# Optimization experiments

Hardware: AMD Instinct MI355X
Metric: run time of the kernel (lower is better)

The kernel has to match this reference:

```python
import jax, jax.numpy as jnp
import numpy as np

FIELD_DIMS = [100000, 50000, 1000, 500, 100, 50, 20, 10]
INPUT_DIM = sum(FIELD_DIMS)            # 151680
NUM_FIELDS = len(FIELD_DIMS)           # 8
FACTOR_DIM = 16
HIDDEN = [256, 128]
OFFSETS = np.concatenate([[0], np.cumsum(FIELD_DIMS)[:-1]]).astype(np.int32)
BATCH = 2048
EPS = 1e-5


def setup_inputs() -> dict:
    key = jax.random.key(0)
    ks = jax.random.split(key, 32)
    # per-field indices, each within its own cardinality
    x = jnp.stack([
        jax.random.randint(ks[f], (BATCH,), 0, FIELD_DIMS[f], dtype=jnp.int32)
        for f in range(NUM_FIELDS)
    ], axis=1)  # [B, F]
    # concatenated embedding tables (xavier_uniform per torch init, approximated with uniform)
    lim = float(np.sqrt(6.0 / (max(FIELD_DIMS) + FACTOR_DIM)))
    emb_table = jax.random.uniform(ks[8], (INPUT_DIM, FACTOR_DIM), minval=-lim, maxval=lim, dtype=jnp.float32)
    # FM linear: weight ~ N(0, 0.01), bias 0
    w_lin = 0.01 * jax.random.normal(ks[9], (INPUT_DIM,), dtype=jnp.float32)
    b_lin = jnp.zeros((), dtype=jnp.float32)
    d0 = NUM_FIELDS * FACTOR_DIM  # 128
    def lin(k, fan_in, fan_out):
        b = float(np.sqrt(1.0 / fan_in))
        kw, kb = jax.random.split(k)
        W = jax.random.uniform(kw, (fan_in, fan_out), minval=-b, maxval=b, dtype=jnp.float32)
        bias = jax.random.uniform(kb, (fan_out,), minval=-b, maxval=b, dtype=jnp.float32)
        return W, bias
    W1, b1 = lin(ks[10], d0, HIDDEN[0])
    W2, b2 = lin(ks[11], HIDDEN[0], HIDDEN[1])
    W3, b3 = lin(ks[12], HIDDEN[1], 1)
    g1 = jnp.ones((HIDDEN[0],), jnp.float32); be1 = jnp.zeros((HIDDEN[0],), jnp.float32)
    g2 = jnp.ones((HIDDEN[1],), jnp.float32); be2 = jnp.zeros((HIDDEN[1],), jnp.float32)
    return {"x": x, "emb_table": emb_table, "w_lin": w_lin, "b_lin": b_lin,
            "W1": W1, "b1": b1, "g1": g1, "be1": be1,
            "W2": W2, "b2": b2, "g2": g2, "be2": be2,
            "W3": W3, "b3": b3}


def _batchnorm(h, gamma, beta):
    # training-mode BN (torch default): biased batch variance
    m = jnp.mean(h, axis=0)
    v = jnp.mean((h - m) ** 2, axis=0)
    return gamma * (h - m) / jnp.sqrt(v + EPS) + beta


def reference(x, emb_table, w_lin, b_lin, W1, b1, g1, be1, W2, b2, g2, be2, W3, b3):
    B = x.shape[0]
    offsets = jnp.asarray(OFFSETS)
    # --- faithful to original bug: scatter one-hot uses RAW x (no field offsets) ---
    sparse_x = jnp.zeros((B, INPUT_DIM), jnp.float32).at[
        jnp.arange(B)[:, None], x].set(1.0)  # duplicates collapse to 1.0, like scatter_
    y_linear = sparse_x @ w_lin + b_lin  # [B]
    # --- dense field embeddings (offset gather into concatenated table) ---
    dense_x = emb_table[x + offsets[None, :]]  # [B, F, K]
    s = jnp.sum(dense_x, axis=1)               # [B, K]
    square_of_sum = s * s
    sum_of_square = jnp.sum(dense_x * dense_x, axis=1)
    y_pairwise = 0.5 * jnp.sum(square_of_sum - sum_of_square, axis=1)  # [B]
    y_fm = y_linear + y_pairwise
    # --- DNN on concatenated embeddings ---
    h = dense_x.reshape(B, NUM_FIELDS * FACTOR_DIM)
    h = jax.nn.relu(_batchnorm(h @ W1 + b1, g1, be1))
    h = jax.nn.relu(_batchnorm(h @ W2 + b2, g2, be2))
    y_dnn = (h @ W3 + b3)[:, 0]  # [B]
    return y_fm + y_dnn
```

## Files before the change

### kernel.cpp

```cpp
#include <hip/hip_runtime.h>

#define EPS 1e-5f

static __device__ const int OFFS[8] = {0, 100000, 150000, 151000, 151500, 151600, 151650, 151670};

__global__ __launch_bounds__(256) void k1_gather_fm_gemm1(
    const int* __restrict__ x, const float* __restrict__ emb,
    const float* __restrict__ wlin, const float* __restrict__ blin,
    const float* __restrict__ W1, const float* __restrict__ b1,
    float* __restrict__ yfm, float* __restrict__ z1, float* __restrict__ p1)
{
    __shared__ __align__(16) float h0s[8][128];
    __shared__ __align__(16) float redS[8][128];
    __shared__ __align__(16) float redQ[8][128];

    const int t = threadIdx.x;
    const int rt = blockIdx.x >> 1, ch = blockIdx.x & 1;

    {
        const int r = t >> 5, c = t & 31;
        const int row = rt * 8 + r;
        const int f = c >> 2, dq = (c & 3) * 4;
        const int idxf = x[row * 8 + f];
        float4 e = *(const float4*)&emb[(size_t)(idxf + OFFS[f]) * 16 + dq];
        *(float4*)&h0s[r][f * 16 + dq] = e;

        if (ch == 0) {
            float4 s = e;
            float4 q = make_float4(e.x * e.x, e.y * e.y, e.z * e.z, e.w * e.w);
#pragma unroll
            for (int m = 4; m <= 16; m <<= 1) {
                s.x += __shfl_xor(s.x, m); s.y += __shfl_xor(s.y, m);
                s.z += __shfl_xor(s.z, m); s.w += __shfl_xor(s.w, m);
                q.x += __shfl_xor(q.x, m); q.y += __shfl_xor(q.y, m);
                q.z += __shfl_xor(q.z, m); q.w += __shfl_xor(q.w, m);
            }
            float pair = (s.x * s.x - q.x) + (s.y * s.y - q.y)
                       + (s.z * s.z - q.z) + (s.w * s.w - q.w);
            pair += __shfl_xor(pair, 1);
            pair += __shfl_xor(pair, 2);

            float lin = 0.f;
            if (c < 8) {
                int ids[8];
#pragma unroll
                for (int g = 0; g < 8; ++g) ids[g] = x[row * 8 + g];
                bool dup = false;
                for (int g = 0; g < c; ++g) dup = dup || (ids[g] == ids[c]);
                lin = dup ? 0.f : wlin[ids[c]];
            }
            lin += __shfl_xor(lin, 1);
            lin += __shfl_xor(lin, 2);
            lin += __shfl_xor(lin, 4);
            if (c == 0) yfm[row] = 0.5f * pair + lin + blin[0];
        }
    }
    __syncthreads();

    const int cc = t & 63, rg = t >> 6;
    const int j = ch * 128 + cc * 2;
    const int r0 = rg * 2;
    float a00 = 0.f, a01 = 0.f, a10 = 0.f, a11 = 0.f;
#pragma unroll
    for (int k0 = 0; k0 < 128; k0 += 16) {
        float4 ha[4], hb[4];
#pragma unroll
        for (int i = 0; i < 4; ++i) {
            ha[i] = *(const float4*)&h0s[r0][k0 + i * 4];
            hb[i] = *(const float4*)&h0s[r0 + 1][k0 + i * 4];
        }
        float2 w[16];
#pragma unroll
        for (int kk = 0; kk < 16; ++kk)
            w[kk] = *(const float2*)&W1[(size_t)(k0 + kk) * 256 + j];
#pragma unroll
        for (int kk = 0; kk < 16; ++kk) {
            const float hva = ((const float*)ha)[kk];
            const float hvb = ((const float*)hb)[kk];
            a00 += hva * w[kk].x; a01 += hva * w[kk].y;
            a10 += hvb * w[kk].x; a11 += hvb * w[kk].y;
        }
    }
    float2 b2v = *(const float2*)&b1[j];
    float z00 = a00 + b2v.x, z01 = a01 + b2v.y;
    float z10 = a10 + b2v.x, z11 = a11 + b2v.y;
    *(float2*)&z1[(size_t)(rt * 8 + r0) * 256 + j]     = make_float2(z00, z01);
    *(float2*)&z1[(size_t)(rt * 8 + r0 + 1) * 256 + j] = make_float2(z10, z11);
    *(float2*)&redS[r0][cc * 2]     = make_float2(z00, z01);
    *(float2*)&redS[r0 + 1][cc * 2] = make_float2(z10, z11);
    *(float2*)&redQ[r0][cc * 2]     = make_float2(z00 * z00, z01 * z01);
    *(float2*)&redQ[r0 + 1][cc * 2] = make_float2(z10 * z10, z11 * z11);
    __syncthreads();
    if (t < 128) {
        float s = 0.f, q = 0.f;
#pragma unroll
        for (int rr = 0; rr < 8; ++rr) { s += redS[rr][t]; q += redQ[rr][t]; }
        *(float2*)&p1[(size_t)(rt * 256 + ch * 128 + t) * 2] = make_float2(s, q);
    }
}

template <int NCOLS>
__global__ __launch_bounds__(256) void kr_stats(
    const float* __restrict__ p, const float* __restrict__ gamma,
    const float* __restrict__ beta, float* __restrict__ sg)
{
    __shared__ float partS[4][8], partQ[4][8];
    const int t = threadIdx.x, blk = blockIdx.x;
    const int cc = t & 7, g = t >> 3;
    const int col = blk * 8 + cc;

    float s = 0.f, q = 0.f;
#pragma unroll
    for (int i = 0; i < 8; ++i) {
        float2 v = *(const float2*)&p[(size_t)((g + i * 32) * NCOLS + col) * 2];
        s += v.x; q += v.y;
    }
#pragma unroll
    for (int m = 8; m <= 32; m <<= 1) {
        s += __shfl_xor(s, m);
        q += __shfl_xor(q, m);
    }
    if ((t & 63) < 8) {
        partS[t >> 6][cc] = s;
        partQ[t >> 6][cc] = q;
    }
    __syncthreads();
    if (t < 8) {
        float fs = partS[0][t] + partS[1][t] + partS[2][t] + partS[3][t];
        float fq = partQ[0][t] + partQ[1][t] + partQ[2][t] + partQ[3][t];
        const int c = blk * 8 + t;
        float mean = fs * (1.f / 2048.f);
        float var  = fq * (1.f / 2048.f) - mean * mean;
        float sc = gamma[c] * __frsqrt_rn(var + EPS);
        sg[c] = sc;
        sg[NCOLS + c] = beta[c] - mean * sc;
    }
}

__global__ __launch_bounds__(512) void k2_bn1_gemm2(
    const float* __restrict__ z1, const float* __restrict__ s1g,
    const float* __restrict__ W2, const float* __restrict__ b2,
    float* __restrict__ z2, float* __restrict__ p2)
{
    __shared__ __align__(16) float h1s[8][256];
    __shared__ __align__(16) float redS[8][128];
    __shared__ __align__(16) float redQ[8][128];

    const int t = threadIdx.x, blk = blockIdx.x;

    {
        const int lr = t >> 6, lc = (t & 63) * 4;
        float4 zv = *(const float4*)&z1[(size_t)(blk * 8 + lr) * 256 + lc];
        float4 sc = *(const float4*)&s1g[lc];
        float4 sh = *(const float4*)&s1g[256 + lc];
        float4 hv;
        hv.x = fmaxf(zv.x * sc.x + sh.x, 0.f);
        hv.y = fmaxf(zv.y * sc.y + sh.y, 0.f);
        hv.z = fmaxf(zv.z * sc.z + sh.z, 0.f);
        hv.w = fmaxf(zv.w * sc.w + sh.w, 0.f);
        *(float4*)&h1s[lr][lc] = hv;
    }
    __syncthreads();

    const int r = t >> 6, j = (t & 63) * 2;
    float a0 = 0.f, a1 = 0.f;
#pragma unroll
    for (int k0 = 0; k0 < 256; k0 += 16) {
        float4 h[4];
#pragma unroll
        for (int i = 0; i < 4; ++i) h[i] = *(const float4*)&h1s[r][k0 + i * 4];
        float2 w[16];
#pragma unroll
        for (int kk = 0; kk < 16; ++kk)
            w[kk] = *(const float2*)&W2[(size_t)(k0 + kk) * 128 + j];
#pragma unroll
        for (int kk = 0; kk < 16; ++kk) {
            const float hv = ((const float*)h)[kk];
            a0 += hv * w[kk].x; a1 += hv * w[kk].y;
        }
    }
    float2 bv = *(const float2*)&b2[j];
    float za = a0 + bv.x, zb = a1 + bv.y;
    *(float2*)&z2[(size_t)(blk * 8 + r) * 128 + j] = make_float2(za, zb);
    *(float2*)&redS[r][j] = make_float2(za, zb);
    *(float2*)&redQ[r][j] = make_float2(za * za, zb * zb);
    __syncthreads();
    if (t < 128) {
        float s = 0.f, q = 0.f;
#pragma unroll
        for (int rr = 0; rr < 8; ++rr) { s += redS[rr][t]; q += redQ[rr][t]; }
        *(float2*)&p2[(size_t)(blk * 128 + t) * 2] = make_float2(s, q);
    }
}

__global__ __launch_bounds__(256) void k3_bn2_out(
    const float* __restrict__ z2, const float* __restrict__ s2g,
    const float* __restrict__ W3, const float* __restrict__ b3,
    const float* __restrict__ yfm, float* __restrict__ out)
{
    const int t = threadIdx.x, blk = blockIdx.x;
    const int r = t >> 5, l = t & 31;
    const int b = blk * 8 + r;
    float4 zv = *(const float4*)&z2[(size_t)b * 128 + l * 4];
    float4 sc = *(const float4*)&s2g[l * 4];
    float4 sh = *(const float4*)&s2g[128 + l * 4];
    float4 wv = *(const float4*)&W3[l * 4];
    float acc = fmaxf(zv.x * sc.x + sh.x, 0.f) * wv.x
              + fmaxf(zv.y * sc.y + sh.y, 0.f) * wv.y
              + fmaxf(zv.z * sc.z + sh.z, 0.f) * wv.z
              + fmaxf(zv.w * sc.w + sh.w, 0.f) * wv.w;
#pragma unroll
    for (int m = 16; m >= 1; m >>= 1) acc += __shfl_xor(acc, m);
    if (l == 0) out[b] = acc + b3[0] + yfm[b];
}

extern "C" void kernel_launch(void* const* d_in, const int* in_sizes, int n_in,
                              void* d_out, int out_size, void* d_ws, size_t ws_size,
                              hipStream_t stream) {
    const int*   x    = (const int*)d_in[0];
    const float* emb  = (const float*)d_in[1];
    const float* wlin = (const float*)d_in[2];
    const float* blin = (const float*)d_in[3];
    const float* W1   = (const float*)d_in[4];
    const float* b1   = (const float*)d_in[5];
    const float* g1   = (const float*)d_in[6];
    const float* be1  = (const float*)d_in[7];
    const float* W2   = (const float*)d_in[8];
    const float* b2   = (const float*)d_in[9];
    const float* g2   = (const float*)d_in[10];
    const float* be2  = (const float*)d_in[11];
    const float* W3   = (const float*)d_in[12];
    const float* b3   = (const float*)d_in[13];

    float* ws  = (float*)d_ws;
    float* yfm = ws;
    float* z1  = yfm + 2048;
    float* p1  = z1 + 2048 * 256;
    float* s1g = p1 + 2 * 256 * 256;
    float* z2  = s1g + 512;
    float* p2  = z2 + 2048 * 128;
    float* s2g = p2 + 2 * 256 * 128;
    float* out = (float*)d_out;

    k1_gather_fm_gemm1<<<512, 256, 0, stream>>>(x, emb, wlin, blin, W1, b1, yfm, z1, p1);
    kr_stats<256><<<32, 256, 0, stream>>>(p1, g1, be1, s1g);
    k2_bn1_gemm2<<<256, 512, 0, stream>>>(z1, s1g, W2, b2, z2, p2);
    kr_stats<128><<<16, 256, 0, stream>>>(p2, g2, be2, s2g);
    k3_bn2_out<<<256, 256, 0, stream>>>(z2, s2g, W3, b3, yfm, out);
}
```

Before: 39.14 us.

## Fuse BN stats and tail kernels into one persistent kernel with grid barriers

Merges the four post-GEMM1 launches into a single 256-block kernel. Each block redundantly reduces the BN1 partial stats itself, and software grid barriers built on per-block atomic flags handle the BN2 stats and the final output. z2 stays in registers instead of going through global memory. The cost is redundant p1 reads in every block and spin-wait barriers, which rely on all 256 blocks being co-resident to avoid deadlock.

```diff
diff --git a/kernel.cpp b/kernel.cpp
--- a/kernel.cpp
+++ b/kernel.cpp
@@ -4,11 +4,42 @@
 
 static __device__ const int OFFS[8] = {0, 100000, 150000, 151000, 151500, 151600, 151650, 151670};
 
-__global__ __launch_bounds__(256) void k1_gather_fm_gemm1(
+__device__ __forceinline__ void st_f2(float* p, float a, float b) {
+    union { float f[2]; unsigned long long u; } v;
+    v.f[0] = a; v.f[1] = b;
+    __hip_atomic_store((unsigned long long*)p, v.u, __ATOMIC_RELAXED, __HIP_MEMORY_SCOPE_AGENT);
+}
+__device__ __forceinline__ float2 ld_f2(const float* p) {
+    union { unsigned long long u; float f[2]; } v;
+    v.u = __hip_atomic_load((const unsigned long long*)p, __ATOMIC_RELAXED, __HIP_MEMORY_SCOPE_AGENT);
+    return make_float2(v.f[0], v.f[1]);
+}
+
+#define BARRIER(ph) do {                                                                   \
+    __syncthreads();                                                                       \
+    if (t == 0)                                                                            \
+        __hip_atomic_store(&flags[blk], (unsigned)(ph),                                    \
+                           __ATOMIC_RELEASE, __HIP_MEMORY_SCOPE_AGENT);                    \
+    if (t < 64) {                                                                          \
+        for (;;) {                                                                         \
+            unsigned f0 = __hip_atomic_load(&flags[t],       __ATOMIC_RELAXED, __HIP_MEMORY_SCOPE_AGENT); \
+            unsigned f1 = __hip_atomic_load(&flags[t + 64],  __ATOMIC_RELAXED, __HIP_MEMORY_SCOPE_AGENT); \
+            unsigned f2 = __hip_atomic_load(&flags[t + 128], __ATOMIC_RELAXED, __HIP_MEMORY_SCOPE_AGENT); \
+            unsigned f3 = __hip_atomic_load(&flags[t + 192], __ATOMIC_RELAXED, __HIP_MEMORY_SCOPE_AGENT); \
+            if (__all(f0 >= (unsigned)(ph) && f1 >= (unsigned)(ph) &&                      \
+                      f2 >= (unsigned)(ph) && f3 >= (unsigned)(ph))) break;                \
+            __builtin_amdgcn_s_sleep(4);                                                   \
+        }                                                                                  \
+    }                                                                                      \
+    __syncthreads();                                                                       \
+} while (0)
+
+__global__ __launch_bounds__(256) void kA_gather_fm_gemm1(
     const int* __restrict__ x, const float* __restrict__ emb,
     const float* __restrict__ wlin, const float* __restrict__ blin,
     const float* __restrict__ W1, const float* __restrict__ b1,
-    float* __restrict__ yfm, float* __restrict__ z1, float* __restrict__ p1)
+    float* __restrict__ yfm, float* __restrict__ z1, float* __restrict__ p1,
+    unsigned* __restrict__ flags)
 {
     __shared__ __align__(16) float h0s[8][128];
     __shared__ __align__(16) float redS[8][128];
@@ -16,6 +47,8 @@
 
     const int t = threadIdx.x;
     const int rt = blockIdx.x >> 1, ch = blockIdx.x & 1;
+
+    if (blockIdx.x == 0) flags[t] = 0;
 
     {
         const int r = t >> 5, c = t & 31;
@@ -99,60 +132,51 @@
     }
 }
 
-template <int NCOLS>
-__global__ __launch_bounds__(256) void kr_stats(
-    const float* __restrict__ p, const float* __restrict__ gamma,
-    const float* __restrict__ beta, float* __restrict__ sg)
-{
-    __shared__ float partS[4][8], partQ[4][8];
-    const int t = threadIdx.x, blk = blockIdx.x;
-    const int cc = t & 7, g = t >> 3;
-    const int col = blk * 8 + cc;
-
-    float s = 0.f, q = 0.f;
-#pragma unroll
-    for (int i = 0; i < 8; ++i) {
-        float2 v = *(const float2*)&p[(size_t)((g + i * 32) * NCOLS + col) * 2];
-        s += v.x; q += v.y;
-    }
-#pragma unroll
-    for (int m = 8; m <= 32; m <<= 1) {
-        s += __shfl_xor(s, m);
-        q += __shfl_xor(q, m);
-    }
-    if ((t & 63) < 8) {
-        partS[t >> 6][cc] = s;
-        partQ[t >> 6][cc] = q;
-    }
-    __syncthreads();
-    if (t < 8) {
-        float fs = partS[0][t] + partS[1][t] + partS[2][t] + partS[3][t];
-        float fq = partQ[0][t] + partQ[1][t] + partQ[2][t] + partQ[3][t];
-        const int c = blk * 8 + t;
-        float mean = fs * (1.f / 2048.f);
-        float var  = fq * (1.f / 2048.f) - mean * mean;
-        float sc = gamma[c] * __frsqrt_rn(var + EPS);
-        sg[c] = sc;
-        sg[NCOLS + c] = beta[c] - mean * sc;
-    }
-}
-
-__global__ __launch_bounds__(512) void k2_bn1_gemm2(
-    const float* __restrict__ z1, const float* __restrict__ s1g,
+__global__ __launch_bounds__(512) void kB_rest(
+    const float* __restrict__ z1, const float* __restrict__ p1,
+    const float* __restrict__ g1, const float* __restrict__ be1,
     const float* __restrict__ W2, const float* __restrict__ b2,
-    float* __restrict__ z2, float* __restrict__ p2)
+    const float* __restrict__ g2, const float* __restrict__ be2,
+    const float* __restrict__ W3, const float* __restrict__ b3,
+    const float* __restrict__ yfm,
+    unsigned* __restrict__ flags, float* __restrict__ p2,
+    float* __restrict__ s2g, float* __restrict__ out)
 {
     __shared__ __align__(16) float h1s[8][256];
-    __shared__ __align__(16) float redS[8][128];
-    __shared__ __align__(16) float redQ[8][128];
+    __shared__ __align__(16) float sclS[256], shfS[256];
+    __shared__ __align__(16) float sbuf[2][256], qbuf[2][256];
+    __shared__ __align__(16) float redS[8][128], redQ[8][128];
+    __shared__ float partS[8][8], partQ[8][8];
 
     const int t = threadIdx.x, blk = blockIdx.x;
+
+    {
+        const int col = t & 255, h = t >> 8;
+        float s = 0.f, q = 0.f;
+#pragma unroll 16
+        for (int i = 0; i < 128; ++i) {
+            float2 v = *(const float2*)&p1[(size_t)((h * 128 + i) * 256 + col) * 2];
+            s += v.x; q += v.y;
+        }
+        sbuf[h][col] = s; qbuf[h][col] = q;
+    }
+    __syncthreads();
+    if (t < 256) {
+        float s = sbuf[0][t] + sbuf[1][t];
+        float q = qbuf[0][t] + qbuf[1][t];
+        float mean = s * (1.f / 2048.f);
+        float var  = q * (1.f / 2048.f) - mean * mean;
+        float sc = g1[t] * __frsqrt_rn(var + EPS);
+        sclS[t] = sc;
+        shfS[t] = be1[t] - mean * sc;
+    }
+    __syncthreads();
 
     {
         const int lr = t >> 6, lc = (t & 63) * 4;
         float4 zv = *(const float4*)&z1[(size_t)(blk * 8 + lr) * 256 + lc];
-        float4 sc = *(const float4*)&s1g[lc];
-        float4 sh = *(const float4*)&s1g[256 + lc];
+        float4 sc = *(const float4*)&sclS[lc];
+        float4 sh = *(const float4*)&shfS[lc];
         float4 hv;
         hv.x = fmaxf(zv.x * sc.x + sh.x, 0.f);
         hv.y = fmaxf(zv.y * sc.y + sh.y, 0.f);
@@ -163,55 +187,82 @@
     __syncthreads();
 
     const int r = t >> 6, j = (t & 63) * 2;
-    float a0 = 0.f, a1 = 0.f;
-#pragma unroll
-    for (int k0 = 0; k0 < 256; k0 += 16) {
-        float4 h[4];
-#pragma unroll
-        for (int i = 0; i < 4; ++i) h[i] = *(const float4*)&h1s[r][k0 + i * 4];
-        float2 w[16];
-#pragma unroll
-        for (int kk = 0; kk < 16; ++kk)
-            w[kk] = *(const float2*)&W2[(size_t)(k0 + kk) * 128 + j];
-#pragma unroll
-        for (int kk = 0; kk < 16; ++kk) {
-            const float hv = ((const float*)h)[kk];
-            a0 += hv * w[kk].x; a1 += hv * w[kk].y;
-        }
-    }
-    float2 bv = *(const float2*)&b2[j];
-    float za = a0 + bv.x, zb = a1 + bv.y;
-    *(float2*)&z2[(size_t)(blk * 8 + r) * 128 + j] = make_float2(za, zb);
-    *(float2*)&redS[r][j] = make_float2(za, zb);
-    *(float2*)&redQ[r][j] = make_float2(za * za, zb * zb);
+    float z2a, z2b;
+    {
+        float a0 = 0.f, a1 = 0.f;
+#pragma unroll
+        for (int k0 = 0; k0 < 256; k0 += 16) {
+            float4 h[4];
+#pragma unroll
+            for (int i = 0; i < 4; ++i) h[i] = *(const float4*)&h1s[r][k0 + i * 4];
+            float2 w[16];
+#pragma unroll
+            for (int kk = 0; kk < 16; ++kk)
+                w[kk] = *(const float2*)&W2[(size_t)(k0 + kk) * 128 + j];
+#pragma unroll
+            for (int kk = 0; kk < 16; ++kk) {
+                const float hv = ((const float*)h)[kk];
+                a0 += hv * w[kk].x; a1 += hv * w[kk].y;
+            }
+        }
+        float2 bv = *(const float2*)&b2[j];
+        z2a = a0 + bv.x; z2b = a1 + bv.y;
+    }
+    *(float2*)&redS[r][j] = make_float2(z2a, z2b);
+    *(float2*)&redQ[r][j] = make_float2(z2a * z2a, z2b * z2b);
     __syncthreads();
     if (t < 128) {
         float s = 0.f, q = 0.f;
 #pragma unroll
         for (int rr = 0; rr < 8; ++rr) { s += redS[rr][t]; q += redQ[rr][t]; }
-        *(float2*)&p2[(size_t)(blk * 128 + t) * 2] = make_float2(s, q);
-    }
-}
-
-__global__ __launch_bounds__(256) void k3_bn2_out(
-    const float* __restrict__ z2, const float* __restrict__ s2g,
-    const float* __restrict__ W3, const float* __restrict__ b3,
-    const float* __restrict__ yfm, float* __restrict__ out)
-{
-    const int t = threadIdx.x, blk = blockIdx.x;
-    const int r = t >> 5, l = t & 31;
-    const int b = blk * 8 + r;
-    float4 zv = *(const float4*)&z2[(size_t)b * 128 + l * 4];
-    float4 sc = *(const float4*)&s2g[l * 4];
-    float4 sh = *(const float4*)&s2g[128 + l * 4];
-    float4 wv = *(const float4*)&W3[l * 4];
-    float acc = fmaxf(zv.x * sc.x + sh.x, 0.f) * wv.x
-              + fmaxf(zv.y * sc.y + sh.y, 0.f) * wv.y
-              + fmaxf(zv.z * sc.z + sh.z, 0.f) * wv.z
-              + fmaxf(zv.w * sc.w + sh.w, 0.f) * wv.w;
-#pragma unroll
-    for (int m = 16; m >= 1; m >>= 1) acc += __shfl_xor(acc, m);
-    if (l == 0) out[b] = acc + b3[0] + yfm[b];
+        st_f2(&p2[(size_t)(blk * 128 + t) * 2], s, q);
+    }
+
+    BARRIER(1);
+
+    if (blk < 16) {
+        const int cc = t & 7, g = t >> 3;
+        const int col = blk * 8 + cc;
+        float s = 0.f, q = 0.f;
+#pragma unroll
+        for (int i = 0; i < 4; ++i) {
+            float2 v = ld_f2(&p2[(size_t)((g + i * 64) * 128 + col) * 2]);
+            s += v.x; q += v.y;
+        }
+#pragma unroll
+        for (int m = 8; m <= 32; m <<= 1) {
+            s += __shfl_xor(s, m);
+            q += __shfl_xor(q, m);
+        }
+        if ((t & 63) < 8) {
+            partS[t >> 6][cc] = s;
+            partQ[t >> 6][cc] = q;
+        }
+        __syncthreads();
+        if (t < 8) {
+            float fs = 0.f, fq = 0.f;
+#pragma unroll
+            for (int w = 0; w < 8; ++w) { fs += partS[w][t]; fq += partQ[w][t]; }
+            const int c = blk * 8 + t;
+            float mean = fs * (1.f / 2048.f);
+            float var  = fq * (1.f / 2048.f) - mean * mean;
+            float sc = g2[c] * __frsqrt_rn(var + EPS);
+            st_f2(&s2g[2 * c], sc, be2[c] - mean * sc);
+        }
+    }
+
+    BARRIER(2);
+
+    {
+        float2 sa = ld_f2(&s2g[2 * j]);
+        float2 sb = ld_f2(&s2g[2 * (j + 1)]);
+        float2 w3 = *(const float2*)&W3[j];
+        float acc = fmaxf(z2a * sa.x + sa.y, 0.f) * w3.x
+                  + fmaxf(z2b * sb.x + sb.y, 0.f) * w3.y;
+#pragma unroll
+        for (int m = 1; m <= 32; m <<= 1) acc += __shfl_xor(acc, m);
+        if ((t & 63) == 0) out[blk * 8 + r] = acc + b3[0] + yfm[blk * 8 + r];
+    }
 }
 
 extern "C" void kernel_launch(void* const* d_in, const int* in_sizes, int n_in,
@@ -236,15 +287,13 @@
     float* yfm = ws;
     float* z1  = yfm + 2048;
     float* p1  = z1 + 2048 * 256;
-    float* s1g = p1 + 2 * 256 * 256;
-    float* z2  = s1g + 512;
-    float* p2  = z2 + 2048 * 128;
+    float* p2  = p1 + 2 * 256 * 256;
     float* s2g = p2 + 2 * 256 * 128;
+    unsigned* flags = (unsigned*)(s2g + 256);
     float* out = (float*)d_out;
 
-    k1_gather_fm_gemm1<<<512, 256, 0, stream>>>(x, emb, wlin, blin, W1, b1, yfm, z1, p1);
-    kr_stats<256><<<32, 256, 0, stream>>>(p1, g1, be1, s1g);
-    k2_bn1_gemm2<<<256, 512, 0, stream>>>(z1, s1g, W2, b2, z2, p2);
-    kr_stats<128><<<16, 256, 0, stream>>>(p2, g2, be2, s2g);
-    k3_bn2_out<<<256, 256, 0, stream>>>(z2, s2g, W3, b3, yfm, out);
-}
+    kA_gather_fm_gemm1<<<512, 256, 0, stream>>>(x, emb, wlin, blin, W1, b1,
+                                                yfm, z1, p1, flags);
+    kB_rest<<<256, 512, 0, stream>>>(z1, p1, g1, be1, W2, b2, g2, be2, W3, b3,
+                                     yfm, flags, p2, s2g, out);
+}
```

After: 54.34 us. 38.8% more time.

## Fold BatchNorm stats reduction into consumer kernels, dropping two launches

Applied to the files above, without the earlier changes.

Removes the two separate kr_stats kernels. Every block of k2 and k3 now redundantly reduces the per-row-tile partial sums from global memory and computes the BN scale and shift into shared memory. This cuts two kernel launches and their dependency gaps. In exchange, each of the 256 blocks rereads the full partial buffer (512 KB for p1, 256 KB for p2) with a serial 128-iteration loop per thread, which adds L2 traffic and latency at the start of each block.

```diff
diff --git a/kernel.cpp b/kernel.cpp
--- a/kernel.cpp
+++ b/kernel.cpp
@@ -99,60 +99,46 @@
     }
 }
 
-template <int NCOLS>
-__global__ __launch_bounds__(256) void kr_stats(
-    const float* __restrict__ p, const float* __restrict__ gamma,
-    const float* __restrict__ beta, float* __restrict__ sg)
-{
-    __shared__ float partS[4][8], partQ[4][8];
-    const int t = threadIdx.x, blk = blockIdx.x;
-    const int cc = t & 7, g = t >> 3;
-    const int col = blk * 8 + cc;
-
-    float s = 0.f, q = 0.f;
-#pragma unroll
-    for (int i = 0; i < 8; ++i) {
-        float2 v = *(const float2*)&p[(size_t)((g + i * 32) * NCOLS + col) * 2];
-        s += v.x; q += v.y;
-    }
-#pragma unroll
-    for (int m = 8; m <= 32; m <<= 1) {
-        s += __shfl_xor(s, m);
-        q += __shfl_xor(q, m);
-    }
-    if ((t & 63) < 8) {
-        partS[t >> 6][cc] = s;
-        partQ[t >> 6][cc] = q;
-    }
-    __syncthreads();
-    if (t < 8) {
-        float fs = partS[0][t] + partS[1][t] + partS[2][t] + partS[3][t];
-        float fq = partQ[0][t] + partQ[1][t] + partQ[2][t] + partQ[3][t];
-        const int c = blk * 8 + t;
-        float mean = fs * (1.f / 2048.f);
-        float var  = fq * (1.f / 2048.f) - mean * mean;
-        float sc = gamma[c] * __frsqrt_rn(var + EPS);
-        sg[c] = sc;
-        sg[NCOLS + c] = beta[c] - mean * sc;
-    }
-}
-
 __global__ __launch_bounds__(512) void k2_bn1_gemm2(
-    const float* __restrict__ z1, const float* __restrict__ s1g,
+    const float* __restrict__ z1, const float* __restrict__ p1,
+    const float* __restrict__ g1, const float* __restrict__ be1,
     const float* __restrict__ W2, const float* __restrict__ b2,
     float* __restrict__ z2, float* __restrict__ p2)
 {
     __shared__ __align__(16) float h1s[8][256];
-    __shared__ __align__(16) float redS[8][128];
-    __shared__ __align__(16) float redQ[8][128];
+    __shared__ __align__(16) float sclS[256], shfS[256];
+    __shared__ __align__(16) float sbuf[2][256], qbuf[2][256];
+    __shared__ __align__(16) float redS[8][128], redQ[8][128];
 
     const int t = threadIdx.x, blk = blockIdx.x;
+
+    {
+        const int col = t & 255, h = t >> 8;
+        float s = 0.f, q = 0.f;
+#pragma unroll 16
+        for (int i = 0; i < 128; ++i) {
+            float2 v = *(const float2*)&p1[(size_t)((h * 128 + i) * 256 + col) * 2];
+            s += v.x; q += v.y;
+        }
+        sbuf[h][col] = s; qbuf[h][col] = q;
+    }
+    __syncthreads();
+    if (t < 256) {
+        float s = sbuf[0][t] + sbuf[1][t];
+        float q = qbuf[0][t] + qbuf[1][t];
+        float mean = s * (1.f / 2048.f);
+        float var  = q * (1.f / 2048.f) - mean * mean;
+        float sc = g1[t] * __frsqrt_rn(var + EPS);
+        sclS[t] = sc;
+        shfS[t] = be1[t] - mean * sc;
+    }
+    __syncthreads();
 
     {
         const int lr = t >> 6, lc = (t & 63) * 4;
         float4 zv = *(const float4*)&z1[(size_t)(blk * 8 + lr) * 256 + lc];
-        float4 sc = *(const float4*)&s1g[lc];
-        float4 sh = *(const float4*)&s1g[256 + lc];
+        float4 sc = *(const float4*)&sclS[lc];
+        float4 sh = *(const float4*)&shfS[lc];
         float4 hv;
         hv.x = fmaxf(zv.x * sc.x + sh.x, 0.f);
         hv.y = fmaxf(zv.y * sc.y + sh.y, 0.f);
@@ -194,16 +180,43 @@
 }
 
 __global__ __launch_bounds__(256) void k3_bn2_out(
-    const float* __restrict__ z2, const float* __restrict__ s2g,
+    const float* __restrict__ z2, const float* __restrict__ p2,
+    const float* __restrict__ g2, const float* __restrict__ be2,
     const float* __restrict__ W3, const float* __restrict__ b3,
     const float* __restrict__ yfm, float* __restrict__ out)
 {
+    __shared__ __align__(16) float sbuf[2][128], qbuf[2][128];
+    __shared__ __align__(16) float scl[128], shf[128];
+
     const int t = threadIdx.x, blk = blockIdx.x;
+
+    {
+        const int col = t & 127, h = t >> 7;
+        float s = 0.f, q = 0.f;
+#pragma unroll 16
+        for (int i = 0; i < 128; ++i) {
+            float2 v = *(const float2*)&p2[(size_t)((h * 128 + i) * 128 + col) * 2];
+            s += v.x; q += v.y;
+        }
+        sbuf[h][col] = s; qbuf[h][col] = q;
+    }
+    __syncthreads();
+    if (t < 128) {
+        float s = sbuf[0][t] + sbuf[1][t];
+        float q = qbuf[0][t] + qbuf[1][t];
+        float mean = s * (1.f / 2048.f);
+        float var  = q * (1.f / 2048.f) - mean * mean;
+        float sc = g2[t] * __frsqrt_rn(var + EPS);
+        scl[t] = sc;
+        shf[t] = be2[t] - mean * sc;
+    }
+    __syncthreads();
+
     const int r = t >> 5, l = t & 31;
     const int b = blk * 8 + r;
     float4 zv = *(const float4*)&z2[(size_t)b * 128 + l * 4];
-    float4 sc = *(const float4*)&s2g[l * 4];
-    float4 sh = *(const float4*)&s2g[128 + l * 4];
+    float4 sc = *(const float4*)&scl[l * 4];
+    float4 sh = *(const float4*)&shf[l * 4];
     float4 wv = *(const float4*)&W3[l * 4];
     float acc = fmaxf(zv.x * sc.x + sh.x, 0.f) * wv.x
               + fmaxf(zv.y * sc.y + sh.y, 0.f) * wv.y
@@ -236,15 +249,11 @@
     float* yfm = ws;
     float* z1  = yfm + 2048;
     float* p1  = z1 + 2048 * 256;
-    float* s1g = p1 + 2 * 256 * 256;
-    float* z2  = s1g + 512;
+    float* z2  = p1 + 2 * 256 * 256;
     float* p2  = z2 + 2048 * 128;
-    float* s2g = p2 + 2 * 256 * 128;
     float* out = (float*)d_out;
 
     k1_gather_fm_gemm1<<<512, 256, 0, stream>>>(x, emb, wlin, blin, W1, b1, yfm, z1, p1);
-    kr_stats<256><<<32, 256, 0, stream>>>(p1, g1, be1, s1g);
-    k2_bn1_gemm2<<<256, 512, 0, stream>>>(z1, s1g, W2, b2, z2, p2);
-    kr_stats<128><<<16, 256, 0, stream>>>(p2, g2, be2, s2g);
-    k3_bn2_out<<<256, 256, 0, stream>>>(z2, s2g, W3, b3, yfm, out);
-}
+    k2_bn1_gemm2<<<256, 512, 0, stream>>>(z1, p1, g1, be1, W2, b2, z2, p2);
+    k3_bn2_out<<<256, 256, 0, stream>>>(z2, p2, g2, be2, W3, b3, yfm, out);
+}
```

New measurement: 48.83 us. +24.7%, slower.
